# Kernel tuning notes

Measured on AMD Instinct MI355X. Metric: run time of the kernel, lower is better.

Reference implementation:

```python
import jax, jax.numpy as jnp
import numpy as np
import math

B, N, DMODEL, H = 8, 1024, 256, 8
HEAD_DIM = DMODEL // H


def setup_inputs() -> dict:
    key = jax.random.key(0)
    ks = jax.random.split(key, 8)
    x = jax.random.normal(ks[0], (B, N, DMODEL), dtype=jnp.float32)
    # symmetric-ish nonnegative pairwise distances
    adj = jax.random.uniform(ks[1], (B, N, N), dtype=jnp.float32) * 10.0
    mask = jax.random.uniform(ks[2], (B, N)) < 0.9  # bool, mostly valid nodes
    W_qkv = jax.random.normal(ks[3], (DMODEL, 3 * DMODEL), dtype=jnp.float32) / math.sqrt(DMODEL)
    b_qkv = jax.random.normal(ks[4], (3 * DMODEL,), dtype=jnp.float32) * 0.01
    shifts = jnp.arange(1.0, H + 1.0, dtype=jnp.float32)  # initial_shifts
    widths = jnp.ones((H,), dtype=jnp.float32)            # initial_widths
    # self_loop_W = 1/head_dim + U(0,1), non-trainable
    self_loop_w = 1.0 / HEAD_DIM + jax.random.uniform(ks[5], (H,), dtype=jnp.float32)
    return {"x": x, "adj": adj, "mask": mask, "W_qkv": W_qkv, "b_qkv": b_qkv,
            "shifts": shifts, "widths": widths, "self_loop_w": self_loop_w}


def reference(x, adj, mask, W_qkv, b_qkv, shifts, widths, self_loop_w):
    b, n, _ = x.shape
    h = shifts.shape[0]
    d = W_qkv.shape[1] // (3 * h)
    qkv = (x @ W_qkv + b_qkv).reshape(b, n, 3, h, d)
    qkv = jnp.transpose(qkv, (2, 0, 3, 1, 4))  # [3, B, H, N, D]
    Q, K, V = qkv[0], qkv[1], qkv[2]
    scores = jnp.einsum('bhnd,bhmd->bhnm', Q, K) / jnp.sqrt(jnp.float32(d))
    # Gaussian moire focus on adjacency distances, per head
    sh = shifts.reshape(1, h, 1, 1)
    w = jnp.maximum(widths, 0.5).reshape(1, h, 1, 1)
    moire = jnp.exp(-((adj[:, None, :, :] - sh) ** 2) / w)
    adjusted = scores + jnp.log(jnp.maximum(moire, 1e-6))
    eye = jnp.eye(n, dtype=adjusted.dtype)  # [N, N]
    adjusted = adjusted + eye * self_loop_w.reshape(1, h, 1, 1)
    mask2d = (mask[:, :, None] & mask[:, None, :])[:, None, :, :]  # [B,1,N,N]
    adjusted = jnp.where(mask2d, adjusted, jnp.float32(-1000000.0))
    attn = jax.nn.softmax(adjusted, axis=-1)
    out = jnp.einsum('bhnm,bhmd->bhnd', attn, V)
    return jnp.transpose(out, (0, 2, 1, 3)).reshape(b, n, h * d)
```

## Files before the change

kernel.cpp:

```cpp
#include <hip/hip_runtime.h>

#define BB 8
#define NN 1024
#define DM 256
#define HH 8
#define HD 32
#define TC 768

typedef __bf16 bf16x8 __attribute__((ext_vector_type(8)));
typedef __bf16 bf16x4 __attribute__((ext_vector_type(4)));
typedef float  f32x4  __attribute__((ext_vector_type(4)));
typedef unsigned int u32;

__global__ __launch_bounds__(256) void precast(
    const float* __restrict__ x, const float* __restrict__ W,
    __bf16* __restrict__ xb, __bf16* __restrict__ Wt)
{
  const int tid = threadIdx.x;
  const int bid = blockIdx.x;
  if (bid < 48) {
    __shared__ __bf16 T[64][65];
    const int ct = bid % 12, kt = bid / 12;
    const int c0 = ct * 64, k0 = kt * 64;
    #pragma unroll
    for (int i = 0; i < 16; ++i) {
      int e = tid + i * 256, kk = e >> 6, cc = e & 63;
      T[cc][kk] = (__bf16)W[(size_t)(k0 + kk) * TC + c0 + cc];
    }
    __syncthreads();
    #pragma unroll
    for (int i = 0; i < 16; ++i) {
      int e = tid + i * 256, cc = e >> 6, kk = e & 63;
      Wt[(size_t)(c0 + cc) * DM + k0 + kk] = T[cc][kk];
    }
  } else {
    const size_t e = (size_t)(bid - 48) * 256 + tid;
    const float4 v = ((const float4*)x)[e];
    bf16x4 o;
    o[0] = (__bf16)v.x; o[1] = (__bf16)v.y;
    o[2] = (__bf16)v.z; o[3] = (__bf16)v.w;
    ((bf16x4*)xb)[e] = o;
  }
}

__global__ __launch_bounds__(256, 3) void qkv_gemm(
    const __bf16* __restrict__ xb, const __bf16* __restrict__ Wt,
    const float* __restrict__ bias, __bf16* __restrict__ Qb,
    __bf16* __restrict__ Kb, __bf16* __restrict__ Vt)
{
  __shared__ __align__(16) char LDSU[49152];
  __bf16* As0 = (__bf16*)LDSU;
  __bf16* Bs0 = (__bf16*)(LDSU + 16384);
  __bf16* As1 = (__bf16*)(LDSU + 24576);
  __bf16* Bs1 = (__bf16*)(LDSU + 40960);

  const int tid  = threadIdx.x;
  const int w    = tid >> 6, lane = tid & 63;
  const int n16  = lane & 15, quad = lane >> 4;
  const int m0   = blockIdx.y * 128, c0 = blockIdx.x * 64;
  const int bb   = m0 >> 10, n0 = m0 & 1023;

  const int stRow = w*8 + (lane >> 3);
  const int stG   = (lane & 7) ^ (lane >> 3);
  const __bf16* gA = &xb[(size_t)(m0 + stRow)*DM + stG*8];
  const __bf16* gB = &Wt[(size_t)(c0 + stRow)*DM + stG*8];

#define QKV_STAGE(Adst, Bdst, K0) do {                                        \
    _Pragma("unroll")                                                         \
    for (int i_ = 0; i_ < 4; ++i_) {                                          \
      const __bf16* gp_ = gA + (size_t)(i_*32)*DM + (K0);                     \
      __bf16* lp_ = (Adst) + (i_*32 + w*8)*64;                                \
      __builtin_amdgcn_global_load_lds(                                       \
          (const __attribute__((address_space(1))) u32*)gp_,                  \
          (__attribute__((address_space(3))) u32*)lp_, 16, 0, 0);             \
    }                                                                         \
    _Pragma("unroll")                                                         \
    for (int i_ = 0; i_ < 2; ++i_) {                                          \
      const __bf16* gp_ = gB + (size_t)(i_*32)*DM + (K0);                     \
      __bf16* lp_ = (Bdst) + (i_*32 + w*8)*64;                                \
      __builtin_amdgcn_global_load_lds(                                       \
          (const __attribute__((address_space(1))) u32*)gp_,                  \
          (__attribute__((address_space(3))) u32*)lp_, 16, 0, 0);             \
    }                                                                         \
  } while (0)

  f32x4 acc[2][4] = {};

  QKV_STAGE(As0, Bs0, 0);
  __syncthreads();

  #pragma unroll
  for (int kk = 0; kk < 4; ++kk) {
    __bf16* Ac = (kk & 1) ? As1 : As0;
    __bf16* Bc = (kk & 1) ? Bs1 : Bs0;
    if (kk == 0)      QKV_STAGE(As1, Bs1, 64);
    else if (kk == 1) QKV_STAGE(As0, Bs0, 128);
    else if (kk == 2) QKV_STAGE(As1, Bs1, 192);
    #pragma unroll
    for (int ks = 0; ks < 2; ++ks) {
      const int ch = ((ks*4 + quad) ^ (n16 & 7)) * 8;
      bf16x8 af0 = *(const bf16x8*)&Ac[(w*32 + n16)*64 + ch];
      bf16x8 af1 = *(const bf16x8*)&Ac[(w*32 + 16 + n16)*64 + ch];
      #pragma unroll
      for (int cb = 0; cb < 4; ++cb) {
        bf16x8 bfb = *(const bf16x8*)&Bc[(cb*16 + n16)*64 + ch];
        acc[0][cb] = __builtin_amdgcn_mfma_f32_16x16x32_bf16(af0, bfb, acc[0][cb], 0, 0, 0);
        acc[1][cb] = __builtin_amdgcn_mfma_f32_16x16x32_bf16(af1, bfb, acc[1][cb], 0, 0, 0);
      }
    }
    __syncthreads();
  }

  float bv[4];
  #pragma unroll
  for (int cb = 0; cb < 4; ++cb) bv[cb] = bias[c0 + cb*16 + n16];

  if (c0 < 512) {
    __bf16* Ct = (__bf16*)LDSU;
    #pragma unroll
    for (int cb = 0; cb < 4; ++cb)
      #pragma unroll
      for (int mb = 0; mb < 2; ++mb)
        #pragma unroll
        for (int r = 0; r < 4; ++r)
          Ct[(w*32 + mb*16 + quad*4 + r)*72 + cb*16 + n16] =
              (__bf16)(acc[mb][cb][r] + bv[cb]);
    __syncthreads();
    const int chunk = tid & 3, hh = (tid >> 2) & 1, rbase = tid >> 3;
    const int c_head = c0 + hh*32;
    const int h = (c_head >> 5) & 7;
    __bf16* base = (c_head >> 8) ? Kb : Qb;
    #pragma unroll
    for (int it = 0; it < 4; ++it) {
      int rl = rbase + it*32;
      bf16x8 v = *(const bf16x8*)&Ct[rl*72 + hh*32 + chunk*8];
      *(bf16x8*)&base[((size_t)((bb*HH + h)*NN + n0 + rl))*HD + chunk*8] = v;
    }
  } else {
    __bf16* CtT = (__bf16*)LDSU;
    #pragma unroll
    for (int cb = 0; cb < 4; ++cb)
      #pragma unroll
      for (int mb = 0; mb < 2; ++mb) {
        bf16x4 t;
        #pragma unroll
        for (int r = 0; r < 4; ++r) t[r] = (__bf16)(acc[mb][cb][r] + bv[cb]);
        *(bf16x4*)&CtT[(cb*16 + n16)*136 + w*32 + mb*16 + quad*4] = t;
      }
    __syncthreads();
    const int col = tid >> 2, sg = tid & 3;
    const int c = c0 + col;
    const int h = (c >> 5) & 7, dd = c & 31;
    __bf16* dst = &Vt[((size_t)((bb*HH + h)*HD + dd))*NN + n0 + sg*32];
    const __bf16* srcp = &CtT[col*136 + sg*32];
    #pragma unroll
    for (int q2 = 0; q2 < 4; ++q2)
      *(bf16x8*)&dst[q2*8] = *(const bf16x8*)&srcp[q2*8];
  }
}

__global__ __launch_bounds__(256, 4) void attn_kernel(
    const __bf16* __restrict__ Q, const __bf16* __restrict__ K,
    const __bf16* __restrict__ Vt, const float* __restrict__ adj,
    const int* __restrict__ mask, const float* __restrict__ shifts,
    const float* __restrict__ widths, const float* __restrict__ slw,
    float* __restrict__ out)
{
  __shared__ __align__(16) char PsU[8192];
  __shared__ __align__(16) __bf16 Ks[2][64][40];
  __shared__ __align__(16) __bf16 Vts[2][32][72];

  const int tid  = threadIdx.x;
  const int w    = tid >> 6, lane = tid & 63;
  const int n16  = lane & 15, quad = lane >> 4;
  const int h    = blockIdx.x >> 7;
  const int lo   = blockIdx.x & 127;
  const int b    = lo >> 4, qt = lo & 15;
  const int bh   = b*8 + h;
  const int q0   = qt * 64;

  const float L2E   = 1.4426950408889634f;
  const float sh    = shifts[h];
  const float ninvw = -L2E / fmaxf(widths[h], 0.5f);
  const float slv   = slw[h] * L2E;
  const float scl   = 0.17677669529663687f * L2E;
  const float MASKV = -28.0f;
  const float c1 = -2.0f * sh * ninvw;
  const float c2 = sh * sh * ninvw;

  const int srow = tid >> 2, sseg = tid & 3;
  const int vd   = tid >> 3, vsg  = tid & 7;

  const __bf16* Kg = K + (size_t)bh*NN*HD;
  const __bf16* Vg = Vt + (size_t)bh*HD*NN;

  const bf16x8 qf =
      *(const bf16x8*)&Q[((size_t)bh*NN + q0 + w*16 + n16)*HD + quad*8];

  {
    *(bf16x8*)&Ks[0][srow][sseg*8] = *(const bf16x8*)&Kg[srow*HD + sseg*8];
    *(bf16x8*)&Vts[0][vd][vsg*8]   = *(const bf16x8*)&Vg[(size_t)vd*NN + vsg*8];
  }
  int mq[4];
  #pragma unroll
  for (int r = 0; r < 4; ++r) mq[r] = mask[b*NN + q0 + w*16 + quad*4 + r];

  const float* arow0 = adj + ((size_t)(b*NN + q0 + w*16 + quad*4))*NN + n16;
  const float* arow1 = arow0 + NN;
  const float* arow2 = arow0 + 2*NN;
  const float* arow3 = arow0 + 3*NN;
  const int*   mrp   = mask + b*NN + n16;

  float av[2][4][4];
  int   mj[2][4];
  #pragma unroll
  for (int cb = 0; cb < 4; ++cb) mj[0][cb] = mrp[cb*16];
  #pragma unroll
  for (int cb = 0; cb < 4; ++cb) {
    av[0][0][cb] = arow0[cb*16];
    av[0][1][cb] = arow1[cb*16];
    av[0][2][cb] = arow2[cb*16];
    av[0][3][cb] = arow3[cb*16];
  }
  arow0 += 64; arow1 += 64; arow2 += 64; arow3 += 64; mrp += 64;

  const int w16q4 = w*16 + quad*4;
  const int hi    = n16 >> 3;
  const int lo2   = (n16 & 7) * 2;
  const int S01   = (w16q4 >> 1) & 7;
  const int S23   = ((w16q4 >> 1) + 1) & 7;
  char* PsW01[4]; char* PsW23[4];
  #pragma unroll
  for (int cb = 0; cb < 4; ++cb) {
    PsW01[cb] = PsU + (size_t)w16q4*128     + ((((2*cb + hi) ^ S01) << 4) + lo2);
    PsW23[cb] = PsU + (size_t)(w16q4+2)*128 + ((((2*cb + hi) ^ S23) << 4) + lo2);
  }
  const int rowR = w*16 + n16;
  const int SR   = (n16 >> 1) & 7;
  const char* PsR0 = PsU + (size_t)rowR*128 + (((quad ^ SR)    ) << 4);
  const char* PsR1 = PsU + (size_t)rowR*128 + (((quad ^ SR) ^ 4) << 4);

  const f32x4 zero = {0.f, 0.f, 0.f, 0.f};
  f32x4 o0 = zero, o1 = zero, lacc = zero;
  bf16x8 onesb;
  #pragma unroll
  for (int i = 0; i < 8; ++i) onesb[i] = (__bf16)1.0f;

  __syncthreads();

  #pragma unroll 2
  for (int jtl = 0; jtl < 16; ++jtl) {
    const int cur = jtl & 1, nxt = cur ^ 1;
    const int j0  = jtl * 64;

    bf16x8 kn, vn;
    if (jtl < 15) {
      kn = *(const bf16x8*)&Kg[(j0 + 64 + srow)*HD + sseg*8];
      vn = *(const bf16x8*)&Vg[(size_t)vd*NN + j0 + 64 + vsg*8];
      #pragma unroll
      for (int cb = 0; cb < 4; ++cb) mj[nxt][cb] = mrp[cb*16];
      #pragma unroll
      for (int cb = 0; cb < 4; ++cb) {
        av[nxt][0][cb] = arow0[cb*16];
        av[nxt][1][cb] = arow1[cb*16];
        av[nxt][2][cb] = arow2[cb*16];
        av[nxt][3][cb] = arow3[cb*16];
      }
      arow0 += 64; arow1 += 64; arow2 += 64; arow3 += 64; mrp += 64;
    }

    f32x4 s[4];
    #pragma unroll
    for (int cb = 0; cb < 4; ++cb) {
      bf16x8 kf = *(const bf16x8*)&Ks[cur][cb*16 + n16][quad*8];
      s[cb] = __builtin_amdgcn_mfma_f32_16x16x32_bf16(qf, kf, zero, 0, 0, 0);
    }

    const bool diagtile = (jtl == qt);
    #pragma unroll
    for (int r = 0; r < 4; ++r) {
      const int rowl = w16q4 + r;
      #pragma unroll
      for (int cb = 0; cb < 4; ++cb) {
        float a   = av[cur][r][cb];
        float mo  = fmaf(a, fmaf(a, ninvw, c1), c2);
        float val = fmaf(s[cb][r], scl, mo);
        if (diagtile && (cb*16 + n16 == rowl)) val += slv;
        bool ok = (mq[r] != 0) && (mj[cur][cb] != 0);
        val = ok ? val : MASKV;
        float p = __builtin_amdgcn_exp2f(val);
        char* wp = (r < 2 ? PsW01[cb] : PsW23[cb]) + (r & 1) * 128;
        *(__bf16*)wp = (__bf16)p;
      }
    }

    bf16x8 a0  = *(const bf16x8*)PsR0;
    bf16x8 a1  = *(const bf16x8*)PsR1;
    bf16x8 b00 = *(const bf16x8*)&Vts[cur][n16][quad*8];
    bf16x8 b01 = *(const bf16x8*)&Vts[cur][n16][32 + quad*8];
    bf16x8 b10 = *(const bf16x8*)&Vts[cur][16 + n16][quad*8];
    bf16x8 b11 = *(const bf16x8*)&Vts[cur][16 + n16][32 + quad*8];
    o0   = __builtin_amdgcn_mfma_f32_16x16x32_bf16(a0, b00, o0, 0, 0, 0);
    o0   = __builtin_amdgcn_mfma_f32_16x16x32_bf16(a1, b01, o0, 0, 0, 0);
    o1   = __builtin_amdgcn_mfma_f32_16x16x32_bf16(a0, b10, o1, 0, 0, 0);
    o1   = __builtin_amdgcn_mfma_f32_16x16x32_bf16(a1, b11, o1, 0, 0, 0);
    lacc = __builtin_amdgcn_mfma_f32_16x16x32_bf16(a0, onesb, lacc, 0, 0, 0);
    lacc = __builtin_amdgcn_mfma_f32_16x16x32_bf16(a1, onesb, lacc, 0, 0, 0);

    if (jtl < 15) {
      *(bf16x8*)&Ks[nxt][srow][sseg*8] = kn;
      *(bf16x8*)&Vts[nxt][vd][vsg*8]   = vn;
    }
    __syncthreads();
  }

  #pragma unroll
  for (int r = 0; r < 4; ++r) {
    const float invl = 1.0f / lacc[r];
    const int n = q0 + w*16 + quad*4 + r;
    float* og = out + ((size_t)(b*NN + n))*DM + h*HD;
    og[n16]      = o0[r] * invl;
    og[16 + n16] = o1[r] * invl;
  }
}

extern "C" void kernel_launch(void* const* d_in, const int* in_sizes, int n_in,
                              void* d_out, int out_size, void* d_ws, size_t ws_size,
                              hipStream_t stream) {
  const float* x      = (const float*)d_in[0];
  const float* adj    = (const float*)d_in[1];
  const int*   mask   = (const int*)d_in[2];
  const float* W      = (const float*)d_in[3];
  const float* bias   = (const float*)d_in[4];
  const float* shifts = (const float*)d_in[5];
  const float* widths = (const float*)d_in[6];
  const float* slwp   = (const float*)d_in[7];
  float* out = (float*)d_out;

  const size_t BHND = (size_t)BB*HH*NN*HD;
  const size_t WTN  = (size_t)TC*DM;
  __bf16* xbuf = (__bf16*)d_ws;
  __bf16* Wt   = xbuf + BHND;
  __bf16* Qb   = Wt + WTN;
  __bf16* Kb   = Qb + BHND;
  __bf16* Vt   = Kb + BHND;

  precast<<<dim3(48 + (int)(BHND/4/256)), 256, 0, stream>>>(x, W, xbuf, Wt);
  qkv_gemm<<<dim3(TC/64, (BB*NN)/128), 256, 0, stream>>>(xbuf, Wt, bias, Qb, Kb, Vt);
  attn_kernel<<<dim3(BB*HH*16), 256, 0, stream>>>(Qb, Kb, Vt, adj, mask,
                                                  shifts, widths, slwp, out);
}
```

Measured before the change: 133.8 us.

## Load K/V fragments directly from global, drop shared staging and block barriers

Measured after the change: 210.0 us. +56.9%, slower.

```diff
diff --git a/kernel.cpp b/kernel.cpp
--- a/kernel.cpp
+++ b/kernel.cpp
@@ -166,17 +166,13 @@
     const float* __restrict__ widths, const float* __restrict__ slw,
     float* __restrict__ out)
 {
-  __shared__ __align__(16) char PsU[8192];
-  __shared__ __align__(16) __bf16 Ks[2][64][40];
-  __shared__ __align__(16) __bf16 Vts[2][32][72];
+  __shared__ __align__(16) __bf16 Ps[64][72];
 
   const int tid  = threadIdx.x;
   const int w    = tid >> 6, lane = tid & 63;
   const int n16  = lane & 15, quad = lane >> 4;
-  const int h    = blockIdx.x >> 7;
-  const int lo   = blockIdx.x & 127;
-  const int b    = lo >> 4, qt = lo & 15;
-  const int bh   = b*8 + h;
+  const int bh   = blockIdx.x >> 4, qt = blockIdx.x & 15;
+  const int b    = bh >> 3, h = bh & 7;
   const int q0   = qt * 64;
 
   const float L2E   = 1.4426950408889634f;
@@ -188,19 +184,16 @@
   const float c1 = -2.0f * sh * ninvw;
   const float c2 = sh * sh * ninvw;
 
-  const int srow = tid >> 2, sseg = tid & 3;
-  const int vd   = tid >> 3, vsg  = tid & 7;
-
   const __bf16* Kg = K + (size_t)bh*NN*HD;
   const __bf16* Vg = Vt + (size_t)bh*HD*NN;
 
+  const __bf16* kfp  = Kg + (size_t)n16*HD + quad*8;
+  const __bf16* vfp0 = Vg + (size_t)n16*NN + quad*8;
+  const __bf16* vfp1 = Vg + (size_t)(16 + n16)*NN + quad*8;
+
   const bf16x8 qf =
       *(const bf16x8*)&Q[((size_t)bh*NN + q0 + w*16 + n16)*HD + quad*8];
 
-  {
-    *(bf16x8*)&Ks[0][srow][sseg*8] = *(const bf16x8*)&Kg[srow*HD + sseg*8];
-    *(bf16x8*)&Vts[0][vd][vsg*8]   = *(const bf16x8*)&Vg[(size_t)vd*NN + vsg*8];
-  }
   int mq[4];
   #pragma unroll
   for (int r = 0; r < 4; ++r) mq[r] = mask[b*NN + q0 + w*16 + quad*4 + r];
@@ -224,39 +217,27 @@
   }
   arow0 += 64; arow1 += 64; arow2 += 64; arow3 += 64; mrp += 64;
 
-  const int w16q4 = w*16 + quad*4;
-  const int hi    = n16 >> 3;
-  const int lo2   = (n16 & 7) * 2;
-  const int S01   = (w16q4 >> 1) & 7;
-  const int S23   = ((w16q4 >> 1) + 1) & 7;
-  char* PsW01[4]; char* PsW23[4];
-  #pragma unroll
-  for (int cb = 0; cb < 4; ++cb) {
-    PsW01[cb] = PsU + (size_t)w16q4*128     + ((((2*cb + hi) ^ S01) << 4) + lo2);
-    PsW23[cb] = PsU + (size_t)(w16q4+2)*128 + ((((2*cb + hi) ^ S23) << 4) + lo2);
-  }
-  const int rowR = w*16 + n16;
-  const int SR   = (n16 >> 1) & 7;
-  const char* PsR0 = PsU + (size_t)rowR*128 + (((quad ^ SR)    ) << 4);
-  const char* PsR1 = PsU + (size_t)rowR*128 + (((quad ^ SR) ^ 4) << 4);
+  bf16x8 kf[4];
+  #pragma unroll
+  for (int cb = 0; cb < 4; ++cb)
+    kf[cb] = *(const bf16x8*)&kfp[(size_t)(cb*16)*HD];
 
   const f32x4 zero = {0.f, 0.f, 0.f, 0.f};
   f32x4 o0 = zero, o1 = zero, lacc = zero;
   bf16x8 onesb;
   #pragma unroll
   for (int i = 0; i < 8; ++i) onesb[i] = (__bf16)1.0f;
-
-  __syncthreads();
 
   #pragma unroll 2
   for (int jtl = 0; jtl < 16; ++jtl) {
     const int cur = jtl & 1, nxt = cur ^ 1;
     const int j0  = jtl * 64;
 
-    bf16x8 kn, vn;
+    bf16x8 kn[4];
     if (jtl < 15) {
-      kn = *(const bf16x8*)&Kg[(j0 + 64 + srow)*HD + sseg*8];
-      vn = *(const bf16x8*)&Vg[(size_t)vd*NN + j0 + 64 + vsg*8];
+      #pragma unroll
+      for (int cb = 0; cb < 4; ++cb)
+        kn[cb] = *(const bf16x8*)&kfp[(size_t)(j0 + 64 + cb*16)*HD];
       #pragma unroll
       for (int cb = 0; cb < 4; ++cb) mj[nxt][cb] = mrp[cb*16];
       #pragma unroll
@@ -269,17 +250,20 @@
       arow0 += 64; arow1 += 64; arow2 += 64; arow3 += 64; mrp += 64;
     }
 
+    bf16x8 b00 = *(const bf16x8*)&vfp0[j0];
+    bf16x8 b01 = *(const bf16x8*)&vfp0[j0 + 32];
+    bf16x8 b10 = *(const bf16x8*)&vfp1[j0];
+    bf16x8 b11 = *(const bf16x8*)&vfp1[j0 + 32];
+
     f32x4 s[4];
     #pragma unroll
-    for (int cb = 0; cb < 4; ++cb) {
-      bf16x8 kf = *(const bf16x8*)&Ks[cur][cb*16 + n16][quad*8];
-      s[cb] = __builtin_amdgcn_mfma_f32_16x16x32_bf16(qf, kf, zero, 0, 0, 0);
-    }
+    for (int cb = 0; cb < 4; ++cb)
+      s[cb] = __builtin_amdgcn_mfma_f32_16x16x32_bf16(qf, kf[cb], zero, 0, 0, 0);
 
     const bool diagtile = (jtl == qt);
     #pragma unroll
     for (int r = 0; r < 4; ++r) {
-      const int rowl = w16q4 + r;
+      const int rowl = w*16 + quad*4 + r;
       #pragma unroll
       for (int cb = 0; cb < 4; ++cb) {
         float a   = av[cur][r][cb];
@@ -289,17 +273,12 @@
         bool ok = (mq[r] != 0) && (mj[cur][cb] != 0);
         val = ok ? val : MASKV;
         float p = __builtin_amdgcn_exp2f(val);
-        char* wp = (r < 2 ? PsW01[cb] : PsW23[cb]) + (r & 1) * 128;
-        *(__bf16*)wp = (__bf16)p;
+        Ps[rowl][cb*16 + n16] = (__bf16)p;
       }
     }
 
-    bf16x8 a0  = *(const bf16x8*)PsR0;
-    bf16x8 a1  = *(const bf16x8*)PsR1;
-    bf16x8 b00 = *(const bf16x8*)&Vts[cur][n16][quad*8];
-    bf16x8 b01 = *(const bf16x8*)&Vts[cur][n16][32 + quad*8];
-    bf16x8 b10 = *(const bf16x8*)&Vts[cur][16 + n16][quad*8];
-    bf16x8 b11 = *(const bf16x8*)&Vts[cur][16 + n16][32 + quad*8];
+    bf16x8 a0 = *(const bf16x8*)&Ps[w*16 + n16][quad*8];
+    bf16x8 a1 = *(const bf16x8*)&Ps[w*16 + n16][32 + quad*8];
     o0   = __builtin_amdgcn_mfma_f32_16x16x32_bf16(a0, b00, o0, 0, 0, 0);
     o0   = __builtin_amdgcn_mfma_f32_16x16x32_bf16(a1, b01, o0, 0, 0, 0);
     o1   = __builtin_amdgcn_mfma_f32_16x16x32_bf16(a0, b10, o1, 0, 0, 0);
@@ -308,10 +287,9 @@
     lacc = __builtin_amdgcn_mfma_f32_16x16x32_bf16(a1, onesb, lacc, 0, 0, 0);
 
     if (jtl < 15) {
-      *(bf16x8*)&Ks[nxt][srow][sseg*8] = kn;
-      *(bf16x8*)&Vts[nxt][vd][vsg*8]   = vn;
-    }
-    __syncthreads();
+      #pragma unroll
+      for (int cb = 0; cb < 4; ++cb) kf[cb] = kn[cb];
+    }
   }
 
   #pragma unroll
```
